# Kernel tuning notes

Measured on AMD Instinct MI355X. Metric: run time of the kernel, lower is better.

Reference implementation:

```python
import math
import jax, jax.numpy as jnp
import numpy as np

B, S, HIDDEN = 1, 4096, 2048
HEADS, KVH = 16, 4
HD = HIDDEN // HEADS            # 128
GROUPS = HEADS // KVH           # 4
CHUNK = 1024                    # ring_attention_chunk_size
BASE = 500000.0
MAXPOS = 131072
ORIG = 8192
BFAST, BSLOW, MSCALE_CFG = 32.0, 1.0, 1.0
SCALING = MAXPOS / ORIG


def _yarn_inv_freq():
    dim = HD
    pos_freqs = BASE ** (np.arange(0, dim, 2, dtype=np.float32) / dim)
    extrap = 1.0 / pos_freqs
    interp = 1.0 / (SCALING * pos_freqs)
    low = max(math.floor(dim * math.log(ORIG / (BFAST * 2 * math.pi)) / (2 * math.log(BASE))), 0)
    high = min(math.ceil(dim * math.log(ORIG / (BSLOW * 2 * math.pi)) / (2 * math.log(BASE))), dim - 1)
    i = np.arange(dim // 2, dtype=np.float32)
    smooth = np.clip((i - low) / max(high - low, 1), 0.0, 1.0)  # i<low -> interp, i>high -> extrap
    inv = (1.0 - smooth) * interp + smooth * extrap
    return jnp.asarray(inv, jnp.float32)

INV_FREQ = _yarn_inv_freq()
MSCALE = (0.1 * math.log(SCALING) + 1.0) * MSCALE_CFG  # scaling > 1


def rotate_half(x):
    x1, x2 = jnp.split(x, 2, axis=-1)
    return jnp.concatenate((-x2, x1), axis=-1)


def ring_attention(q, k, v, chunk, causal=True):
    # q,k,v: [B,H,S,D]; kv_len divisible by chunk
    b, h, s, d = q.shape
    kv_len = k.shape[2]
    nc = kv_len // chunk
    scale = d ** (-0.5)
    k_chunks = jnp.moveaxis(k.reshape(b, h, nc, chunk, d), 2, 0)  # [nc,B,H,chunk,D]
    v_chunks = jnp.moveaxis(v.reshape(b, h, nc, chunk, d), 2, 0)
    kv_starts = jnp.arange(nc) * chunk
    q_idx = jnp.arange(s)[:, None]
    k_off = jnp.arange(chunk)[None, :]
    neg_inf = jnp.float32(-jnp.inf)

    def step(carry, inp):
        out, mx, se = carry
        kch, vch, kv_start = inp
        scores = jnp.einsum('bhqd,bhkd->bhqk', q, kch) * scale
        if causal:
            mask = (kv_start + k_off) > q_idx  # [S, chunk]
            scores = jnp.where(mask[None, None], neg_inf, scores)
        chunk_max = scores.max(axis=-1, keepdims=True)
        new_max = jnp.maximum(mx, chunk_max)
        exp_old = se * jnp.exp(mx - new_max)
        exp_chunk = jnp.exp(scores - new_max)
        exp_sum_chunk = exp_chunk.sum(axis=-1, keepdims=True)
        denom = exp_old + exp_sum_chunk + 1e-10
        out = out * (se / denom) + jnp.einsum('bhqk,bhkd->bhqd', exp_chunk, vch) / denom
        return (out, new_max, exp_old + exp_sum_chunk), None

    init = (jnp.zeros_like(q),
            jnp.full((b, h, s, 1), -jnp.inf, dtype=q.dtype),
            jnp.zeros((b, h, s, 1), dtype=q.dtype))
    (out, _, _), _ = jax.lax.scan(step, init, (k_chunks, v_chunks, kv_starts))
    return out


def setup_inputs() -> dict:
    key = jax.random.key(0)
    ks = jax.random.split(key, 5)
    hidden_states = jax.random.normal(ks[0], (B, S, HIDDEN), dtype=jnp.float32)
    position_ids = jnp.broadcast_to(jnp.arange(S, dtype=jnp.int32)[None, :], (B, S))
    sd = 1.0 / math.sqrt(HIDDEN)
    Wq = jax.random.normal(ks[1], (HIDDEN, HEADS * HD), dtype=jnp.float32) * sd
    Wk = jax.random.normal(ks[2], (HIDDEN, KVH * HD), dtype=jnp.float32) * sd
    Wv = jax.random.normal(ks[3], (HIDDEN, KVH * HD), dtype=jnp.float32) * sd
    Wo = jax.random.normal(ks[4], (HEADS * HD, HIDDEN), dtype=jnp.float32) * sd
    return {'hidden_states': hidden_states, 'position_ids': position_ids,
            'Wq': Wq, 'Wk': Wk, 'Wv': Wv, 'Wo': Wo}


def reference(hidden_states, position_ids, Wq, Wk, Wv, Wo):
    b, s, _ = hidden_states.shape
    q = (hidden_states @ Wq).reshape(b, s, HEADS, HD).transpose(0, 2, 1, 3)
    k = (hidden_states @ Wk).reshape(b, s, KVH, HD).transpose(0, 2, 1, 3)
    v = (hidden_states @ Wv).reshape(b, s, KVH, HD).transpose(0, 2, 1, 3)
    # YaRN rope
    freqs = position_ids.astype(jnp.float32)[:, :, None] * INV_FREQ[None, None, :]  # [B,S,HD/2]
    emb = jnp.concatenate((freqs, freqs), axis=-1)  # [B,S,HD]
    cos = (jnp.cos(emb) * MSCALE)[:, None]  # [B,1,S,HD]
    sin = (jnp.sin(emb) * MSCALE)[:, None]
    q = q * cos + rotate_half(q) * sin
    k = k * cos + rotate_half(k) * sin
    # GQA expand
    k = jnp.repeat(k, GROUPS, axis=1)
    v = jnp.repeat(v, GROUPS, axis=1)
    # ring path: use_ring_attention and kv_len > chunk
    attn = ring_attention(q, k, v, CHUNK, causal=True)
    attn = attn.transpose(0, 2, 1, 3).reshape(b, s, HEADS * HD)
    return attn @ Wo
```

## Files before the change

### kernel.cpp

```cpp
#include <hip/hip_runtime.h>
#include <cstdint>
#include <cstddef>


typedef unsigned short u16;
typedef unsigned int u32;
typedef float f32x4 __attribute__((ext_vector_type(4)));
typedef __bf16 bf16x8 __attribute__((ext_vector_type(8)));

__device__ __forceinline__ u16 f2bf(float f) {
    union { float f; u32 u; } v; v.f = f;
    u32 u = v.u;
    u += 0x7fffu + ((u >> 16) & 1u);
    return (u16)(u >> 16);
}
__device__ __forceinline__ float bf2f(u16 b) {
    union { u32 u; float f; } v; v.u = ((u32)b) << 16;
    return v.f;
}
__device__ __forceinline__ u16 f2h(float f) {
    union { _Float16 h; u16 u; } v; v.h = (_Float16)f; return v.u;
}
__device__ __forceinline__ float h2f(u16 u) {
    union { u16 u; _Float16 h; } v; v.u = u; return (float)v.h;
}
__device__ __forceinline__ u32 pkbf(float lo, float hi) {
    union { __bf16 h[2]; u32 u; } v;
    v.h[0] = (__bf16)lo; v.h[1] = (__bf16)hi;
    return v.u;
}
__device__ __forceinline__ float exp2_hw(float x) {
    float r;
    asm("v_exp_f32 %0, %1" : "=v"(r) : "v"(x));
    return r;
}

__device__ __forceinline__ void load16_to_lds(const void* g, void* l) {
    __builtin_amdgcn_global_load_lds((const __attribute__((address_space(1))) u32*)g,
                                     (__attribute__((address_space(3))) u32*)l,
                                     16, 0, 0);
}

#define PIPE_FENCE() do {                                        \
    __builtin_amdgcn_sched_barrier(0);                           \
    asm volatile("s_waitcnt vmcnt(0) lgkmcnt(0)" ::: "memory");  \
    __builtin_amdgcn_sched_barrier(0);                           \
    __builtin_amdgcn_s_barrier();                                \
    __builtin_amdgcn_sched_barrier(0);                           \
} while (0)

#define MFMA16(a, b, c) __builtin_amdgcn_mfma_f32_16x16x32_bf16((a), (b), (c), 0, 0, 0)

__global__ __launch_bounds__(256) void convert_f32_bf16(const float* __restrict__ X,
                                                        u16* __restrict__ Y) {
    const int base = (blockIdx.x * 1024 + threadIdx.x) * 4;
#pragma unroll
    for (int k = 0; k < 4; ++k) {
        const int i = base + k * 1024;
        const float4 v = *(const float4*)(X + i);
        union { u16 s[4]; uint2 u; } pk;
        pk.s[0] = f2bf(v.x); pk.s[1] = f2bf(v.y); pk.s[2] = f2bf(v.z); pk.s[3] = f2bf(v.w);
        *(uint2*)(Y + i) = pk.u;
    }
}

__global__ __launch_bounds__(256) void transpose_w4(const float* __restrict__ Wq,
                                                    const float* __restrict__ Wk,
                                                    const float* __restrict__ Wv,
                                                    const float* __restrict__ Wo,
                                                    u16* __restrict__ Wt,
                                                    u16* __restrict__ Wot) {
    __shared__ float tile[64][65];
    const int bx = blockIdx.x;
    const float* W; u16* dst; int N, n0;
    if (bx < 32)      { W = Wq; dst = Wt;                          N = 2048; n0 = bx * 64; }
    else if (bx < 40) { W = Wk; dst = Wt + (size_t)2048 * 2048;    N = 512;  n0 = (bx - 32) * 64; }
    else if (bx < 48) { W = Wv; dst = Wt + (size_t)2560 * 2048;    N = 512;  n0 = (bx - 40) * 64; }
    else              { W = Wo; dst = Wot;                         N = 2048; n0 = (bx - 48) * 64; }
    const int k0 = blockIdx.y * 64;
    const int tc = threadIdx.x & 63, tr = threadIdx.x >> 6;
#pragma unroll
    for (int i = 0; i < 64; i += 4)
        tile[tc][tr + i] = W[(size_t)(k0 + tr + i) * N + n0 + tc];
    __syncthreads();
#pragma unroll
    for (int i = 0; i < 64; i += 4)
        dst[(size_t)(n0 + tr + i) * 2048 + k0 + tc] = f2bf(tile[tr + i][tc]);
}

__device__ __forceinline__ void store_out(float* p, float v) { *p = v; }
__device__ __forceinline__ void store_out(u16* p, float v) { *p = f2bf(v); }

template <typename OutT>
__global__ __launch_bounds__(256) void gemm_bt(const u16* __restrict__ A,
                                               const u16* __restrict__ Bt,
                                               OutT* __restrict__ C,
                                               int M, int N, int K) {
    __shared__ __align__(16) u16 sA[8192];
    __shared__ __align__(16) u16 sB[8192];
    const int t = threadIdx.x;
    const int lane = t & 63, w = t >> 6;
    const int quad = lane >> 4, l15 = lane & 15;
    const int m0 = blockIdx.x << 7, n0 = blockIdx.y << 7;
    const int wr4 = (w >> 1) * 4, wc4 = (w & 1) * 4;
    f32x4 acc[4][4] = {};
    for (int k0 = 0; k0 < K; k0 += 64) {
        __syncthreads();
#pragma unroll
        for (int r = 0; r < 2; ++r) {
            const int f = w * 2 + r;
#pragma unroll
            for (int kc = 0; kc < 2; ++kc) {
                load16_to_lds(A + (size_t)(m0 + f * 16 + l15) * K + k0 + kc * 32 + quad * 8,
                              sA + (f * 2 + kc) * 512);
                load16_to_lds(Bt + (size_t)(n0 + f * 16 + l15) * K + k0 + kc * 32 + quad * 8,
                              sB + (f * 2 + kc) * 512);
            }
        }
        __syncthreads();
#pragma unroll
        for (int kc = 0; kc < 2; ++kc) {
            bf16x8 af[4], bb[4];
#pragma unroll
            for (int i = 0; i < 4; ++i)
                af[i] = *(const bf16x8*)(sA + ((wr4 + i) * 2 + kc) * 512 + lane * 8);
#pragma unroll
            for (int j = 0; j < 4; ++j)
                bb[j] = *(const bf16x8*)(sB + ((wc4 + j) * 2 + kc) * 512 + lane * 8);
#pragma unroll
            for (int i = 0; i < 4; ++i)
#pragma unroll
                for (int j = 0; j < 4; ++j)
                    acc[i][j] = MFMA16(af[i], bb[j], acc[i][j]);
        }
    }
#pragma unroll
    for (int i = 0; i < 4; ++i)
#pragma unroll
        for (int j = 0; j < 4; ++j) {
            const int row = m0 + (w >> 1) * 64 + i * 16 + quad * 4;
            const int col = n0 + (w & 1) * 64 + j * 16 + l15;
#pragma unroll
            for (int r = 0; r < 4; ++r)
                store_out(C + (size_t)(row + r) * N + col, acc[i][j][r]);
        }
}

__global__ __launch_bounds__(256) void rope_vt_kernel(u16* __restrict__ QKV,
                                                      u16* __restrict__ Vt,
                                                      const int* __restrict__ pos_ids) {
    __shared__ u16 tile[64 * 72];
    if (blockIdx.x >= 5120) {
        const int b = blockIdx.x - 5120;
        const int k0 = (b & 63) * 64, d0 = ((b >> 6) & 1) * 64, kvh = b >> 7;
        const int t = threadIdx.x;
#pragma unroll
        for (int k = 0; k < 4; ++k) {
            const int u = t + k * 256;
            const int key = u >> 4, dg = u & 15;
            const uint2 v = *(const uint2*)(QKV + (size_t)(k0 + key) * 3072 + 2560 + kvh * 128 + d0 + dg * 4);
            *(uint2*)(tile + key * 72 + dg * 4) = v;
        }
        __syncthreads();
#pragma unroll
        for (int k = 0; k < 4; ++k) {
            const int u = t + k * 256;
            const int d = u >> 4, kg = u & 15;
            union { u16 s[4]; uint2 v; } pk;
#pragma unroll
            for (int i = 0; i < 4; ++i) pk.s[i] = tile[(kg * 4 + i) * 72 + d];
            *(uint2*)(Vt + (size_t)(kvh * 128 + d0 + d) * 4096 + k0 + kg * 4) = pk.v;
        }
        return;
    }
    const int u = blockIdx.x * 256 + threadIdx.x;
    const int NQ4 = 4096 * 16 * 16;
    u16* p;
    int s, i4;
    if (u < NQ4) {
        s = u >> 8;
        const int rest = u & 255;
        const int h = rest >> 4;
        i4 = rest & 15;
        p = QKV + (size_t)s * 3072 + h * 128 + i4 * 4;
    } else {
        const int u2 = u - NQ4;
        s = u2 >> 6;
        const int rest = u2 & 63;
        const int h = rest >> 4;
        i4 = rest & 15;
        p = QKV + (size_t)s * 3072 + 2048 + h * 128 + i4 * 4;
    }
    const float pf = (float)pos_ids[s];
    const float MS = 1.2772588722239781f;
    union { u16 s4[4]; uint2 v; } lo, hi, so, sh;
    lo.v = *(const uint2*)(p);
    hi.v = *(const uint2*)(p + 64);
#pragma unroll
    for (int e = 0; e < 4; ++e) {
        const float fi = (float)(i4 * 4 + e);
        const float inv_ex = exp2_hw(fi * -0.29580637f);
        const float inv_in = inv_ex * (1.0f / 16.0f);
        const float sm = fminf(fmaxf((fi - 18.0f) * (1.0f / 17.0f), 0.0f), 1.0f);
        const float inv = (1.0f - sm) * inv_in + sm * inv_ex;
        const float ph = pf * inv;
        const float cs = __cosf(ph) * MS, sn = __sinf(ph) * MS;
        const float x1 = bf2f(lo.s4[e]), x2 = bf2f(hi.s4[e]);
        so.s4[e] = f2bf(x1 * cs - x2 * sn);
        sh.s4[e] = f2bf(x2 * cs + x1 * sn);
    }
    *(uint2*)(p) = so.v;
    *(uint2*)(p + 64) = sh.v;
}

__device__ __forceinline__ void stage_kv(const u16* __restrict__ QKV,
                                         const u16* __restrict__ Vt,
                                         int kt0, int kvh, int w, int l15, int quad,
                                         u16* bK, u16* bV) {
    const u16* gk = QKV + (size_t)(kt0 + w * 16 + l15) * 3072 + 2048 + kvh * 128 + quad * 8;
#pragma unroll
    for (int kc = 0; kc < 4; ++kc)
        load16_to_lds(gk + kc * 32, bK + (w * 4 + kc) * 512);
#pragma unroll
    for (int r = 0; r < 4; ++r) {
        const int dt = w * 2 + (r >> 1), ks = r & 1;
        load16_to_lds(Vt + (size_t)(kvh * 128 + dt * 16 + l15) * 4096 + kt0 + ks * 32 + quad * 8,
                      bV + (dt * 2 + ks) * 512);
    }
}

__global__ __launch_bounds__(256, 2) void attn_partial(const u16* __restrict__ QKV,
                                                       const u16* __restrict__ Vt,
                                                       u16* __restrict__ part,
                                                       float* __restrict__ ml) {
    __shared__ __align__(16) u16 sK[2][8192];
    __shared__ __align__(16) u16 sV[2][8192];

    const int t = threadIdx.x;
    const int lane = t & 63, w = t >> 6;
    const int quad = lane >> 4, l15 = lane & 15;
    const int bid = blockIdx.x;
    const int u = bid >> 4, h = bid & 15, kvh = h >> 2;

    int qb, c;
    if (u < 8)       { qb = 8 + u; c = 0; }
    else if (u < 24) { const int r = u - 8;  qb = 16 + (r >> 1); c = r & 1; }
    else if (u < 48) { const int r = u - 24; const int q3 = r / 3; qb = 24 + q3; c = r - q3 * 3; }
    else             { const int r = u - 48; const int k = r >> 2; const int g0 = r & 3;
                       qb = g0 * 8 + (7 - k); c = g0; }
    const int g = qb >> 3;
    const int q0 = qb << 7, kv0 = c << 10;
    const int jmax = (c == g) ? (2 * (qb & 7) + 2) : 16;

    {
        u16* dst0 = (w < 2) ? sK[0] : sV[0];
        const int fbase = (w & 1) * 8;
#pragma unroll
        for (int idx = 0; idx < 8; ++idx) {
            const int qg = idx >> 2, kc = idx & 3;
            load16_to_lds(QKV + (size_t)(q0 + w * 32 + qg * 16 + l15) * 3072 + h * 128 + kc * 32 + quad * 8,
                          dst0 + (fbase + idx) * 512);
        }
    }
    PIPE_FENCE();
    bf16x8 af[2][4];
    {
        const u16* src0 = (w < 2) ? sK[0] : sV[0];
        const int fbase = (w & 1) * 8;
#pragma unroll
        for (int qg = 0; qg < 2; ++qg)
#pragma unroll
            for (int kc = 0; kc < 4; ++kc)
                af[qg][kc] = *(const bf16x8*)(src0 + (fbase + qg * 4 + kc) * 512 + lane * 8);
    }
    stage_kv(QKV, Vt, kv0, kvh, w, l15, quad, sK[1], sV[1]);
    PIPE_FENCE();

    float m_c[2] = {-1e30f, -1e30f}, l_c[2] = {0.0f, 0.0f};
    f32x4 o_c[8][2] = {};
    const float SCALE = 0.08838834764831845f;
    const float LOG2E = 1.4426950408889634f;
    const float CS = SCALE * LOG2E;

    const int srcLo = ((quad & 1) << 5) | l15;
    const int srcHi = srcLo | 16;
    const bool selB = (quad & 2) != 0;

    int cur = 1;
    for (int j = 0; j < jmax; ++j) {
        if (j + 1 < jmax)
            stage_kv(QKV, Vt, kv0 + ((j + 1) << 6), kvh, w, l15, quad,
                     sK[cur ^ 1], sV[cur ^ 1]);

        const u16* bK = sK[cur];
        const u16* bV = sV[cur];
        const int kt0 = kv0 + (j << 6);

        f32x4 sacc[4][2] = {};
#pragma unroll
        for (int j4 = 0; j4 < 4; ++j4)
#pragma unroll
            for (int kc = 0; kc < 4; ++kc) {
                const bf16x8 kf = *(const bf16x8*)(bK + (j4 * 4 + kc) * 512 + lane * 8);
                sacc[j4][0] = MFMA16(kf, af[0][kc], sacc[j4][0]);
                sacc[j4][1] = MFMA16(kf, af[1][kc], sacc[j4][1]);
            }

        const bool diag = (c == g) && ((j >> 1) == (qb & 7));
        if (diag) {
#pragma unroll
            for (int j4 = 0; j4 < 4; ++j4)
#pragma unroll
                for (int qg = 0; qg < 2; ++qg) {
                    const int qrow = q0 + w * 32 + qg * 16 + l15;
#pragma unroll
                    for (int r = 0; r < 4; ++r) {
                        const int key = kt0 + j4 * 16 + quad * 4 + r;
                        if (key > qrow) sacc[j4][qg][r] = -1e30f;
                    }
                }
        }

        bf16x8 pf[2][2];
#pragma unroll
        for (int qg = 0; qg < 2; ++qg) {
            f32x4 v01, v23;
#pragma unroll
            for (int r = 0; r < 4; ++r) {
                v01[r] = fmaxf(sacc[0][qg][r], sacc[1][qg][r]);
                v23[r] = fmaxf(sacc[2][qg][r], sacc[3][qg][r]);
            }
            float mx = fmaxf(fmaxf(fmaxf(v01[0], v01[1]), fmaxf(v01[2], v01[3])),
                             fmaxf(fmaxf(v23[0], v23[1]), fmaxf(v23[2], v23[3])));
            mx = fmaxf(mx, __shfl_xor(mx, 16, 64));
            mx = fmaxf(mx, __shfl_xor(mx, 32, 64));
            const float mn = fmaxf(m_c[qg], mx * SCALE);
            const float alpha = exp2_hw((m_c[qg] - mn) * LOG2E);
            const float kk = -mn * LOG2E;
#pragma unroll
            for (int j4 = 0; j4 < 4; ++j4)
#pragma unroll
                for (int r = 0; r < 4; ++r)
                    sacc[j4][qg][r] = exp2_hw(fmaf(sacc[j4][qg][r], CS, kk));
            const f32x4 pv = (sacc[0][qg] + sacc[1][qg]) + (sacc[2][qg] + sacc[3][qg]);
            float ps = (pv[0] + pv[1]) + (pv[2] + pv[3]);
            ps += __shfl_xor(ps, 16, 64);
            ps += __shfl_xor(ps, 32, 64);
            l_c[qg] = l_c[qg] * alpha + ps;
            m_c[qg] = mn;
#pragma unroll
            for (int dt = 0; dt < 8; ++dt) o_c[dt][qg] *= alpha;

            u32 pk[4][2];
#pragma unroll
            for (int j4 = 0; j4 < 4; ++j4) {
                pk[j4][0] = pkbf(sacc[j4][qg][0], sacc[j4][qg][1]);
                pk[j4][1] = pkbf(sacc[j4][qg][2], sacc[j4][qg][3]);
            }
#pragma unroll
            for (int ks = 0; ks < 2; ++ks) {
                union { u32 wd[4]; bf16x8 v; } bu;
                const u32 a0 = pk[2 * ks][0], a1 = pk[2 * ks][1];
                const u32 b0 = pk[2 * ks + 1][0], b1 = pk[2 * ks + 1][1];
                const u32 xa0 = (u32)__shfl((int)a0, srcLo, 64);
                const u32 xb0 = (u32)__shfl((int)b0, srcLo, 64);
                bu.wd[0] = selB ? xb0 : xa0;
                const u32 xa1 = (u32)__shfl((int)a1, srcLo, 64);
                const u32 xb1 = (u32)__shfl((int)b1, srcLo, 64);
                bu.wd[1] = selB ? xb1 : xa1;
                const u32 ya0 = (u32)__shfl((int)a0, srcHi, 64);
                const u32 yb0 = (u32)__shfl((int)b0, srcHi, 64);
                bu.wd[2] = selB ? yb0 : ya0;
                const u32 ya1 = (u32)__shfl((int)a1, srcHi, 64);
                const u32 yb1 = (u32)__shfl((int)b1, srcHi, 64);
                bu.wd[3] = selB ? yb1 : ya1;
                pf[qg][ks] = bu.v;
            }
        }

#pragma unroll
        for (int ks = 0; ks < 2; ++ks) {
#pragma unroll
            for (int dt = 0; dt < 8; ++dt) {
                const bf16x8 vf = *(const bf16x8*)(bV + (dt * 2 + ks) * 512 + lane * 8);
                o_c[dt][0] = MFMA16(vf, pf[0][ks], o_c[dt][0]);
                o_c[dt][1] = MFMA16(vf, pf[1][ks], o_c[dt][1]);
            }
        }

        if (j + 1 < jmax) {
            PIPE_FENCE();
            cur ^= 1;
        }
    }

#pragma unroll
    for (int qg = 0; qg < 2; ++qg) {
        const float invl = 1.0f / l_c[qg];
        const int q = w * 32 + qg * 16 + l15;
        u16* pbase = part + (size_t)bid * 16384 + (size_t)q * 128 + quad * 4;
#pragma unroll
        for (int dt = 0; dt < 8; ++dt) {
            union { u16 s[4]; uint2 v; } pk4;
#pragma unroll
            for (int r = 0; r < 4; ++r) pk4.s[r] = f2h(o_c[dt][qg][r] * invl);
            *(uint2*)(pbase + dt * 16) = pk4.v;
        }
        if (quad == 0) {
            ml[(size_t)bid * 256 + q * 2] = m_c[qg];
            ml[(size_t)bid * 256 + q * 2 + 1] = l_c[qg];
        }
    }
}

__global__ __launch_bounds__(256) void attn_merge(const u16* __restrict__ part,
                                                  const float* __restrict__ ml,
                                                  u16* __restrict__ attn) {
    const int b = blockIdx.x;
    const int qb = b >> 4, h = b & 15;
    const int g = qb >> 3;
    const int t = threadIdx.x;
    const int slot = t & 15;
    const int qrow = blockIdx.y * 16 + (t >> 4);
    const int d0 = slot * 8;

    float o[8];
#pragma unroll
    for (int i = 0; i < 8; ++i) o[i] = 0.0f;
    float m_g = -1e30f, l_g = 0.0f;

    for (int c = 0; c <= g; ++c) {
        int u;
        if (c == g)      u = 48 + (7 - (qb & 7)) * 4 + g;
        else if (g == 1) u = qb - 8;
        else if (g == 2) u = 8 + (qb - 16) * 2 + c;
        else             u = 24 + (qb - 24) * 3 + c;
        const int tile = u * 16 + h;
        const float m_c = ml[(size_t)tile * 256 + qrow * 2];
        const float l_c = ml[(size_t)tile * 256 + qrow * 2 + 1];
        const float mn = fmaxf(m_g, m_c);
        const float a = l_g * __expf(m_g - mn);
        const float eC = __expf(m_c - mn);
        const float sE = l_c * eC;
        const float d = a + sE + 1e-10f;
        const float f_old = l_g / d;
        const float f_new = sE / d;
        union { u16 s[8]; uint4 v; } ld;
        ld.v = *(const uint4*)(part + (size_t)tile * 16384 + (size_t)qrow * 128 + d0);
#pragma unroll
        for (int jj = 0; jj < 8; ++jj)
            o[jj] = o[jj] * f_old + h2f(ld.s[jj]) * f_new;
        l_g = a + sE;
        m_g = mn;
    }

    union { u16 s[8]; uint4 v; } pk;
#pragma unroll
    for (int i = 0; i < 8; ++i) pk.s[i] = f2bf(o[i]);
    *(uint4*)(attn + (size_t)(qb * 128 + qrow) * 2048 + h * 128 + d0) = pk.v;
}

extern "C" void kernel_launch(void* const* d_in, const int* in_sizes, int n_in,
                              void* d_out, int out_size, void* d_ws, size_t ws_size,
                              hipStream_t stream) {
    const float* X  = (const float*)d_in[0];
    const int* pos  = (const int*)d_in[1];
    const float* Wq = (const float*)d_in[2];
    const float* Wk = (const float*)d_in[3];
    const float* Wv = (const float*)d_in[4];
    const float* Wo = (const float*)d_in[5];
    float* out = (float*)d_out;
    char* ws = (char*)d_ws;

    u16*   part = (u16*)(ws);
    u16*   Xbf  = (u16*)(ws);
    u16*   Wt   = (u16*)(ws + 16777216);
    u16*   QKV  = (u16*)(ws + 41943040);
    u16*   attn = (u16*)(ws + 41943040);
    u16*   Vt   = (u16*)(ws + 67108864);
    float* ml   = (float*)(ws + 71303168);
    u16*   Wot  = (u16*)(ws + 72613888);

    convert_f32_bf16<<<2048, 256, 0, stream>>>(X, Xbf);
    transpose_w4<<<dim3(80, 32), 256, 0, stream>>>(Wq, Wk, Wv, Wo, Wt, Wot);

    gemm_bt<u16><<<dim3(32, 24), 256, 0, stream>>>(Xbf, Wt, QKV, 4096, 3072, 2048);

    rope_vt_kernel<<<5632, 256, 0, stream>>>(QKV, Vt, pos);

    attn_partial<<<1280, 256, 0, stream>>>(QKV, Vt, part, ml);
    attn_merge<<<dim3(512, 8), 256, 0, stream>>>(part, ml, attn);

    gemm_bt<float><<<dim3(32, 16), 256, 0, stream>>>(attn, Wot, out, 4096, 2048, 2048);
}
```

Measured before the change: 426.2 us.

## Double-buffer LDS tiles in bf16 GEMM to overlap loads with MFMA

Reworks the GEMM main loop to keep two LDS buffers of K=32 slices. The next slice is prefetched while MFMAs run on the current one, and the two syncthreads per iteration become a single PIPE_FENCE. This aims to hide global-to-LDS latency behind compute, at the cost of halving the K depth per iteration and doubling the number of loop iterations and fences.

Result: faster. 416.6 us (-2.3%).

```diff
diff --git a/kernel.cpp b/kernel.cpp
--- a/kernel.cpp
+++ b/kernel.cpp
@@ -96,42 +96,54 @@
                                                const u16* __restrict__ Bt,
                                                OutT* __restrict__ C,
                                                int M, int N, int K) {
-    __shared__ __align__(16) u16 sA[8192];
-    __shared__ __align__(16) u16 sB[8192];
+    __shared__ __align__(16) u16 sA[2][4096];
+    __shared__ __align__(16) u16 sB[2][4096];
     const int t = threadIdx.x;
     const int lane = t & 63, w = t >> 6;
     const int quad = lane >> 4, l15 = lane & 15;
     const int m0 = blockIdx.x << 7, n0 = blockIdx.y << 7;
     const int wr4 = (w >> 1) * 4, wc4 = (w & 1) * 4;
     f32x4 acc[4][4] = {};
-    for (int k0 = 0; k0 < K; k0 += 64) {
-        __syncthreads();
-#pragma unroll
-        for (int r = 0; r < 2; ++r) {
-            const int f = w * 2 + r;
-#pragma unroll
-            for (int kc = 0; kc < 2; ++kc) {
-                load16_to_lds(A + (size_t)(m0 + f * 16 + l15) * K + k0 + kc * 32 + quad * 8,
-                              sA + (f * 2 + kc) * 512);
-                load16_to_lds(Bt + (size_t)(n0 + f * 16 + l15) * K + k0 + kc * 32 + quad * 8,
-                              sB + (f * 2 + kc) * 512);
+
+#pragma unroll
+    for (int r = 0; r < 2; ++r) {
+        const int f = w * 2 + r;
+        load16_to_lds(A + (size_t)(m0 + f * 16 + l15) * K + quad * 8, sA[1] + f * 512);
+        load16_to_lds(Bt + (size_t)(n0 + f * 16 + l15) * K + quad * 8, sB[1] + f * 512);
+    }
+    PIPE_FENCE();
+
+    int cur = 1;
+    const int nk = K >> 5;
+    for (int kt = 0; kt < nk; ++kt) {
+        if (kt + 1 < nk) {
+            const int koff = (kt + 1) << 5;
+#pragma unroll
+            for (int r = 0; r < 2; ++r) {
+                const int f = w * 2 + r;
+                load16_to_lds(A + (size_t)(m0 + f * 16 + l15) * K + koff + quad * 8,
+                              sA[cur ^ 1] + f * 512);
+                load16_to_lds(Bt + (size_t)(n0 + f * 16 + l15) * K + koff + quad * 8,
+                              sB[cur ^ 1] + f * 512);
             }
         }
-        __syncthreads();
-#pragma unroll
-        for (int kc = 0; kc < 2; ++kc) {
-            bf16x8 af[4], bb[4];
-#pragma unroll
-            for (int i = 0; i < 4; ++i)
-                af[i] = *(const bf16x8*)(sA + ((wr4 + i) * 2 + kc) * 512 + lane * 8);
+        const u16* bA = sA[cur];
+        const u16* bB = sB[cur];
+        bf16x8 af[4], bb[4];
+#pragma unroll
+        for (int i = 0; i < 4; ++i)
+            af[i] = *(const bf16x8*)(bA + (wr4 + i) * 512 + lane * 8);
+#pragma unroll
+        for (int j = 0; j < 4; ++j)
+            bb[j] = *(const bf16x8*)(bB + (wc4 + j) * 512 + lane * 8);
+#pragma unroll
+        for (int i = 0; i < 4; ++i)
 #pragma unroll
             for (int j = 0; j < 4; ++j)
-                bb[j] = *(const bf16x8*)(sB + ((wc4 + j) * 2 + kc) * 512 + lane * 8);
-#pragma unroll
-            for (int i = 0; i < 4; ++i)
-#pragma unroll
-                for (int j = 0; j < 4; ++j)
-                    acc[i][j] = MFMA16(af[i], bb[j], acc[i][j]);
+                acc[i][j] = MFMA16(af[i], bb[j], acc[i][j]);
+        if (kt + 1 < nk) {
+            PIPE_FENCE();
+            cur ^= 1;
         }
     }
 #pragma unroll
```
